# Performance work log

Measured on AMD Instinct MI355X. Metric: run time of the kernel, lower is better.

Reference implementation:

```python
import jax, jax.numpy as jnp
import numpy as np

G = 256        # graphs per batch
N = 256        # nodes per graph (max_n for dense padding)
D = 256        # node_hidden_dim
H = 8          # num_heads
EPS = 1e-5


def _layer_norm(h, g, b):
    mu = jnp.mean(h, axis=-1, keepdims=True)
    var = jnp.mean((h - mu) ** 2, axis=-1, keepdims=True)
    return (h - mu) * jax.lax.rsqrt(var + EPS) * g + b


def setup_inputs() -> dict:
    key = jax.random.key(0)
    ks = jax.random.split(key, 16)
    s = 0.02
    inp = {
        "x": jax.random.normal(ks[0], (G * N, D), dtype=jnp.float32),
        "batch": jnp.repeat(jnp.arange(G, dtype=jnp.int32), N),  # sorted segment ids
        "batch_CLS": jax.random.normal(ks[1], (G, 1, D), dtype=jnp.float32),
        "Wq": jax.random.normal(ks[2], (D, D), dtype=jnp.float32) * s,
        "bq": jnp.zeros((D,), jnp.float32),
        "Wk": jax.random.normal(ks[3], (D, D), dtype=jnp.float32) * s,
        "bk": jnp.zeros((D,), jnp.float32),
        "Wv": jax.random.normal(ks[4], (D, D), dtype=jnp.float32) * s,
        "bv": jnp.zeros((D,), jnp.float32),
        "Wo": jax.random.normal(ks[5], (D, D), dtype=jnp.float32) * s,
        "bo": jnp.zeros((D,), jnp.float32),
        "g0": jnp.ones((D,), jnp.float32),
        "beta0": jnp.zeros((D,), jnp.float32),
        "W1": jax.random.normal(ks[6], (D, 2 * D), dtype=jnp.float32) * s,
        "b1": jnp.zeros((2 * D,), jnp.float32),
        "W2": jax.random.normal(ks[7], (2 * D, D), dtype=jnp.float32) * s,
        "b2": jnp.zeros((D,), jnp.float32),
        "g1": jnp.ones((D,), jnp.float32),
        "beta1": jnp.zeros((D,), jnp.float32),
    }
    return inp


def reference(x, batch, batch_CLS, Wq, bq, Wk, bk, Wv, bv, Wo, bo,
              g0, beta0, W1, b1, W2, b2, g1, beta1):
    total = x.shape[0]
    batch = batch.astype(jnp.int32)

    # ---- to_dense_batch: scatter nodes into [G, N, D] padded tensor + mask
    counts = jax.ops.segment_sum(jnp.ones((total,), jnp.int32), batch, num_segments=G)
    start = jnp.concatenate([jnp.zeros((1,), jnp.int32), jnp.cumsum(counts)[:-1]])
    pos = jnp.arange(total, dtype=jnp.int32) - start[batch]  # position within graph
    x_dense = jnp.zeros((G, N, D), x.dtype).at[batch, pos].set(x)
    mask = jnp.zeros((G, N), bool).at[batch, pos].set(True)

    # ---- append CLS token per graph
    x_dense = jnp.concatenate([x_dense, batch_CLS], axis=1)            # [G, N+1, D]
    attn_mask = jnp.concatenate([mask, jnp.ones((G, 1), bool)], axis=1)  # [G, N+1]

    # ---- masked multi-head self-attention (split/cat pattern == head reshape)
    dh = D // H
    Q = (x_dense @ Wq + bq).reshape(G, N + 1, H, dh)
    K = (x_dense @ Wk + bk).reshape(G, N + 1, H, dh)
    V = (x_dense @ Wv + bv).reshape(G, N + 1, H, dh)
    scores = jnp.einsum('bqhd,bkhd->bhqk', Q, K) / np.sqrt(dh).astype(np.float32)
    inf_mask = jnp.where(attn_mask, 0.0, -1e9)[:, None, None, :]        # [G,1,1,N+1]
    A = jax.nn.softmax(scores + inf_mask, axis=-1)
    attn = jnp.einsum('bhqk,bkhd->bqhd', A, V).reshape(G, N + 1, D)
    attn = attn @ Wo + bo

    # ---- residual, split CLS back off, gather dense->sparse
    attn = attn + x_dense
    cls = attn[:, -1, :]                       # [G, D]
    nodes = attn[:, :-1, :][batch, pos]        # [total, D] (inverse of to_dense_batch)
    h = jnp.concatenate([nodes, cls], axis=0)  # [total + G, D]

    h = _layer_norm(h, g0, beta0)
    f = jax.nn.relu(h @ W1 + b1) @ W2 + b2
    out = _layer_norm(f + h, g1, beta1)
    return out
```

## Files before the change

kernel.cpp:

```cpp
#include <hip/hip_runtime.h>

typedef __attribute__((ext_vector_type(8))) short short8;
typedef __attribute__((ext_vector_type(8))) unsigned short ushort8;
typedef __attribute__((ext_vector_type(4))) unsigned short ushort4v;
typedef __attribute__((ext_vector_type(4))) float f32x4;
typedef unsigned short ushort;
typedef unsigned int uint;

#define QSCALE 0.17677669529663687f

__device__ __forceinline__ ushort f2bf(float f) {
  union { float f; unsigned u; } a; a.f = f;
  unsigned r = a.u + 0x7fffu + ((a.u >> 16) & 1u);
  return (ushort)(r >> 16);
}
__device__ __forceinline__ float bf2f(ushort u) {
  union { uint u; float f; } a; a.u = ((uint)u) << 16; return a.f;
}
__device__ __forceinline__ uint cvtpk(float a, float b) {
  uint r; asm("v_cvt_pk_bf16_f32 %0, %1, %2" : "=v"(r) : "v"(a), "v"(b)); return r;
}

__device__ __forceinline__ void gload16(const void* g, void* l) {
  __builtin_amdgcn_global_load_lds((const __attribute__((address_space(1))) void*)g,
                                   (__attribute__((address_space(3))) void*)l, 16, 0, 0);
}

__device__ __forceinline__ uint xcd_swz(uint hwid, uint nwg) {
  const uint q8 = nwg >> 3, r8 = nwg & 7;
  const uint xcd = hwid & 7, i8 = hwid >> 3;
  return (xcd < r8 ? xcd * (q8 + 1) : r8 * (q8 + 1) + (xcd - r8) * q8) + i8;
}

__global__ __launch_bounds__(256) void seg_start_k(const int* __restrict__ batch,
                                                   int* __restrict__ start) {
  const int i = blockIdx.x * 256 + threadIdx.x;
  const int b = batch[i];
  if (i == 0 || batch[i - 1] != b) start[b] = i;
  if (i == 0) start[256] = 65536;
}

__global__ __launch_bounds__(256) void prep_w_k(
    const float* __restrict__ Wq, const float* __restrict__ Wk,
    const float* __restrict__ Wv, const float* __restrict__ Wo,
    const float* __restrict__ W1, const float* __restrict__ W2,
    ushort* __restrict__ Wt) {
  const int w = blockIdx.y;
  const float* src; ushort* dst; int Kd, Nd; float sc = 1.0f;
  switch (w) {
    case 0: src = Wq; dst = Wt;          Kd = 256; Nd = 256; sc = QSCALE; break;
    case 1: src = Wk; dst = Wt + 65536;  Kd = 256; Nd = 256; break;
    case 2: src = Wv; dst = Wt + 131072; Kd = 256; Nd = 256; break;
    case 3: src = Wo; dst = Wt + 196608; Kd = 256; Nd = 256; break;
    case 4: src = W1; dst = Wt + 262144; Kd = 256; Nd = 512; break;
    default: src = W2; dst = Wt + 393216; Kd = 512; Nd = 256; break;
  }
  const int e = blockIdx.x * 256 + threadIdx.x;
  if (e < Kd * Nd) {
    const int k = e / Nd, n = e - k * Nd;
    dst[n * Kd + k] = f2bf(src[e] * sc);
  }
}

__global__ __launch_bounds__(256) void pack_xd_k(
    const float* __restrict__ x, const float* __restrict__ cls,
    const int* __restrict__ start, ushort* __restrict__ xd) {
  const size_t idx = (((size_t)blockIdx.x << 8) + threadIdx.x) << 3;
  const int row = (int)(idx >> 8);
  const int col = (int)(idx & 255);
  const int g = row / 257, n = row - g * 257;
  const int sg = start[g], cn = start[g + 1] - sg;
  float4 a, b;
  if (n < cn) {
    const float* src = x + (((size_t)(sg + n)) << 8) + col;
    a = ((const float4*)src)[0]; b = ((const float4*)src)[1];
  } else if (n == 256) {
    const float* src = cls + (((size_t)g) << 8) + col;
    a = ((const float4*)src)[0]; b = ((const float4*)src)[1];
  } else {
    a.x = a.y = a.z = a.w = 0.f; b = a;
  }
  ushort8 o;
  o[0] = f2bf(a.x); o[1] = f2bf(a.y); o[2] = f2bf(a.z); o[3] = f2bf(a.w);
  o[4] = f2bf(b.x); o[5] = f2bf(b.y); o[6] = f2bf(b.z); o[7] = f2bf(b.w);
  *(ushort8*)(xd + idx) = o;
}

template<int EPI>
__device__ __forceinline__ void gemm_a_body(
    const ushort* __restrict__ A, const ushort* __restrict__ Bt,
    int N, int K,
    const float* __restrict__ b0, const float* __restrict__ b1, const float* __restrict__ b2,
    ushort* __restrict__ o0, ushort* __restrict__ o1, ushort* __restrict__ o2,
    float* __restrict__ of32, const ushort* __restrict__ resid,
    const int* __restrict__ start) {
  __shared__ __align__(16) char As[16384];
  __shared__ __align__(16) char Bs[16384];
  const int tid = threadIdx.x, lane = tid & 63, wid = tid >> 6;
  const int hi = lane >> 4, lc = lane & 15;
  const int wm = wid >> 1, wn = wid & 1;

  const uint nx = gridDim.x, ny = gridDim.y;
  const uint hwid = blockIdx.y * nx + blockIdx.x;
  const uint wg = xcd_swz(hwid, nx * ny);
  const int bx = wg / ny, by = wg % ny;

  const int m0 = bx * 128;
  const int z = (EPI == 0) ? (by >> 1) : 0;
  const int ncol0 = (EPI == 0) ? (by & 1) * 128 : by * 128;
  const ushort* Bz = (EPI == 0) ? Bt + (size_t)z * 65536 : Bt;
  const float* bias = (EPI == 0) ? (z == 0 ? b0 : (z == 1 ? b1 : b2)) : b0;
  const float bmul = (EPI == 0 && z == 0) ? QSCALE : 1.0f;
  ushort* obf = (EPI == 0) ? (z == 0 ? o0 : (z == 1 ? o1 : o2)) : o0;

  f32x4 acc[4][4];
#pragma unroll
  for (int a = 0; a < 4; ++a)
#pragma unroll
    for (int b = 0; b < 4; ++b) acc[a][b] = (f32x4)0.0f;

  for (int kt = 0; kt < K; kt += 64) {
#pragma unroll
    for (int r = 0; r < 4; ++r) {
      const int L = (r * 256 + tid) * 16;
      const int row = L >> 7;
      const int cb = (L & 127) ^ ((row & 7) << 4);
      gload16(A + (size_t)(m0 + row) * K + kt + (cb >> 1), As + L);
    }
#pragma unroll
    for (int r = 0; r < 4; ++r) {
      const int L = (r * 256 + tid) * 16;
      const int row = L >> 7;
      const int cb = (L & 127) ^ ((row & 7) << 4);
      gload16(Bz + (size_t)(ncol0 + row) * K + kt + (cb >> 1), Bs + L);
    }
    asm volatile("s_waitcnt vmcnt(0)" ::: "memory");
    __syncthreads();
#pragma unroll
    for (int ks = 0; ks < 2; ++ks) {
      short8 af[4], bfr[4];
      const int cB = (ks * 32 + hi * 8) * 2;
#pragma unroll
      for (int t = 0; t < 4; ++t) {
        const int rA = wm * 64 + t * 16 + lc;
        af[t] = *(const short8*)(As + (rA << 7) + (cB ^ ((rA & 7) << 4)));
        const int rB = wn * 64 + t * 16 + lc;
        bfr[t] = *(const short8*)(Bs + (rB << 7) + (cB ^ ((rB & 7) << 4)));
      }
#pragma unroll
      for (int mt = 0; mt < 4; ++mt)
#pragma unroll
        for (int nt = 0; nt < 4; ++nt)
          acc[mt][nt] = __builtin_amdgcn_mfma_f32_16x16x32_bf16(af[mt], bfr[nt], acc[mt][nt], 0, 0, 0);
    }
    __syncthreads();
  }

#pragma unroll
  for (int mt = 0; mt < 4; ++mt)
#pragma unroll
    for (int i = 0; i < 4; ++i) {
      const int m = m0 + wm * 64 + mt * 16 + hi * 4 + i;
      size_t r2 = (size_t)m;
      bool wr = true;
      if constexpr (EPI == 4) {
        const int gg = m / 257, nr = m - gg * 257;
        const int sg = start[gg], cn = start[gg + 1] - sg;
        if (nr < cn) r2 = (size_t)(sg + nr);
        else if (nr == 256) r2 = (size_t)(65536 + gg);
        else wr = false;
      }
#pragma unroll
      for (int nt = 0; nt < 4; ++nt) {
        const int n = ncol0 + wn * 64 + nt * 16 + lc;
        if constexpr (EPI == 0) {
          obf[(size_t)m * N + n] = f2bf(acc[mt][nt][i] + bias[n] * bmul);
        } else if constexpr (EPI == 2) {
          obf[(size_t)m * N + n] = f2bf(fmaxf(acc[mt][nt][i] + bias[n], 0.0f));
        } else if constexpr (EPI == 4) {
          if (wr) {
            const float v = acc[mt][nt][i] + bias[n] + bf2f(resid[((size_t)m << 8) + n]);
            obf[(r2 << 8) + n] = f2bf(v);
          }
        } else {
          const float v = acc[mt][nt][i] + bias[n] + bf2f(resid[((size_t)m << 8) + n]);
          of32[((size_t)m << 8) + n] = v;
        }
      }
    }
}

__global__ __launch_bounds__(256) void gemm_qkv(
    const ushort* A, const ushort* Bt, const float* bq, const float* bk, const float* bv,
    ushort* Q, ushort* K, ushort* V) {
  gemm_a_body<0>(A, Bt, 256, 256, bq, bk, bv, Q, K, V, nullptr, nullptr, nullptr);
}
__global__ __launch_bounds__(256) void gemm_ffn1(
    const ushort* A, const ushort* Bt, const float* b1, ushort* t16) {
  gemm_a_body<2>(A, Bt, 512, 256, b1, nullptr, nullptr, t16, nullptr, nullptr,
                 nullptr, nullptr, nullptr);
}
__global__ __launch_bounds__(256) void gemm_wo(
    const ushort* A, const ushort* Bt, const float* bo,
    ushort* hpre16, const ushort* resid, const int* start) {
  gemm_a_body<4>(A, Bt, 256, 256, bo, nullptr, nullptr, hpre16, nullptr, nullptr,
                 nullptr, resid, start);
}
__global__ __launch_bounds__(256) void gemm_ffn2(
    const ushort* A, const ushort* Bt, const float* b2,
    float* out, const ushort* resid) {
  gemm_a_body<5>(A, Bt, 256, 512, b2, nullptr, nullptr, nullptr, nullptr, nullptr,
                 out, resid, nullptr);
}

template<int IN_BF, int OUT_BF>
__global__ __launch_bounds__(512) void ln_k(const void* __restrict__ in,
                                            const float* __restrict__ gamma,
                                            const float* __restrict__ beta,
                                            void* __restrict__ outp) {
  const int lane = threadIdx.x & 63, wid = threadIdx.x >> 6;
  const size_t r = (size_t)blockIdx.x * 8 + wid;
  float f[4];
  if constexpr (IN_BF) {
    const ushort4v v = *(const ushort4v*)((const ushort*)in + (r << 8) + lane * 4);
    f[0] = bf2f(v[0]); f[1] = bf2f(v[1]); f[2] = bf2f(v[2]); f[3] = bf2f(v[3]);
  } else {
    const float4 v = *(const float4*)((const float*)in + (r << 8) + lane * 4);
    f[0] = v.x; f[1] = v.y; f[2] = v.z; f[3] = v.w;
  }
  float s = (f[0] + f[1]) + (f[2] + f[3]);
  float ss = (f[0] * f[0] + f[1] * f[1]) + (f[2] * f[2] + f[3] * f[3]);
#pragma unroll
  for (int m = 1; m < 64; m <<= 1) {
    s += __shfl_xor(s, m); ss += __shfl_xor(ss, m);
  }
  const float mu = s * (1.0f / 256.0f);
  const float rs = rsqrtf(ss * (1.0f / 256.0f) - mu * mu + 1e-5f);
  const float4 gv = *(const float4*)(gamma + lane * 4);
  const float4 bv = *(const float4*)(beta + lane * 4);
  float o[4];
  o[0] = (f[0] - mu) * rs * gv.x + bv.x;
  o[1] = (f[1] - mu) * rs * gv.y + bv.y;
  o[2] = (f[2] - mu) * rs * gv.z + bv.z;
  o[3] = (f[3] - mu) * rs * gv.w + bv.w;
  if constexpr (OUT_BF) {
    ushort4v u;
    u[0] = f2bf(o[0]); u[1] = f2bf(o[1]); u[2] = f2bf(o[2]); u[3] = f2bf(o[3]);
    *(ushort4v*)((ushort*)outp + (r << 8) + lane * 4) = u;
  } else {
    float4 u; u.x = o[0]; u.y = o[1]; u.z = o[2]; u.w = o[3];
    *(float4*)((float*)outp + (r << 8) + lane * 4) = u;
  }
}

#define KSTR 40
#define VSTR 296
#define OSTR 40
__global__ __launch_bounds__(512) void attn_k(
    const ushort* __restrict__ Q, const ushort* Kb,
    const ushort* __restrict__ Vb, const int* __restrict__ start,
    ushort* O) {
  __shared__ __align__(16) ushort Ks[272 * KSTR];
  __shared__ __align__(16) ushort Vt[32 * VSTR];
  __shared__ __align__(16) ushort Ot[8][16 * OSTR];
  const int tid = threadIdx.x, lane = tid & 63, wid = tid >> 6;
  const int hi = lane >> 4, lo = lane & 15;
  const uint wg = xcd_swz(blockIdx.x, 2048);
  const int g = wg >> 3, h = wg & 7;
  const int cnt = start[g + 1] - start[g];
  const size_t base = ((size_t)g * 257) * 256 + h * 32;

  for (int n = tid; n < 272; n += 512) {
    const bool rv = (n < cnt) || (n == 256);
    if (n < 257 && rv) {
      const ushort* src = Kb + base + ((size_t)n << 8);
#pragma unroll
      for (int j = 0; j < 4; ++j)
        *(ushort8*)(Ks + n * KSTR + j * 8) = *(const ushort8*)(src + j * 8);
    } else {
      const ushort8 zz = (ushort8)0;
#pragma unroll
      for (int j = 0; j < 4; ++j) *(ushort8*)(Ks + n * KSTR + j * 8) = zz;
    }
  }
  for (int it = tid; it < 1152; it += 512) {
    const int n = it >> 2, d0 = (it & 3) * 8;
    const bool rv = (n < cnt) || (n == 256);
    ushort8 v8;
    if (n < 257 && rv) v8 = *(const ushort8*)(Vb + base + ((size_t)n << 8) + d0);
    else v8 = (ushort8)0;
#pragma unroll
    for (int j = 0; j < 8; ++j) Vt[(d0 + j) * VSTR + n] = v8[j];
  }
  __syncthreads();

  for (int qt = wid; qt < 17; qt += 8) {
    const int qr = qt * 16 + lo;
    const int qc = qr < 257 ? qr : 256;
    const short8 qf = *(const short8*)(Q + base + ((size_t)qc << 8) + hi * 8);

    float den = -(float)(271 - cnt);
    uint ds_[17][2];
#pragma unroll
    for (int kt = 0; kt < 17; ++kt) {
      const short8 kf = *(const short8*)(Ks + (kt * 16 + lo) * KSTR + hi * 8);
      const f32x4 st = __builtin_amdgcn_mfma_f32_16x16x32_bf16(kf, qf, (f32x4)0.0f, 0, 0, 0);
      const float e0 = __expf(st[0]), e1 = __expf(st[1]);
      const float e2 = __expf(st[2]), e3 = __expf(st[3]);
      den += (e0 + e1) + (e2 + e3);
      ds_[kt][0] = cvtpk(e0, e1);
      ds_[kt][1] = cvtpk(e2, e3);
    }
    den += __shfl_xor(den, 16);
    den += __shfl_xor(den, 32);
    const float inv = 1.0f / den;

    f32x4 ot0 = (f32x4)0.0f, ot1 = (f32x4)0.0f;
#pragma unroll
    for (int ks = 0; ks < 9; ++ks) {
      union { uint u[4]; short8 s8; } pb;
#pragma unroll
      for (int jp = 0; jp < 4; ++jp) {
        const int sl = lo | ((((hi & 1) << 1) | (jp >> 1)) << 4);
        if (ks < 8) {
          const uint a = (uint)__shfl((int)ds_[2 * ks][jp & 1], sl);
          const uint b = (uint)__shfl((int)ds_[2 * ks + 1][jp & 1], sl);
          pb.u[jp] = (hi < 2) ? a : b;
        } else {
          const uint a = (uint)__shfl((int)ds_[16][jp & 1], sl);
          pb.u[jp] = (hi < 2) ? a : 0u;
        }
      }
      const short8 va0 = *(const short8*)(Vt + lo * VSTR + ks * 32 + hi * 8);
      const short8 va1 = *(const short8*)(Vt + (16 + lo) * VSTR + ks * 32 + hi * 8);
      ot0 = __builtin_amdgcn_mfma_f32_16x16x32_bf16(va0, pb.s8, ot0, 0, 0, 0);
      ot1 = __builtin_amdgcn_mfma_f32_16x16x32_bf16(va1, pb.s8, ot1, 0, 0, 0);
    }

    {
      const uint w0 = cvtpk(ot0[0] * inv, ot0[1] * inv);
      const uint w1 = cvtpk(ot0[2] * inv, ot0[3] * inv);
      const uint w2 = cvtpk(ot1[0] * inv, ot1[1] * inv);
      const uint w3 = cvtpk(ot1[2] * inv, ot1[3] * inv);
      ushort* ob = Ot[wid] + lo * OSTR + hi * 4;
      *(uint*)(ob + 0) = w0;
      *(uint*)(ob + 2) = w1;
      *(uint*)(ob + 16) = w2;
      *(uint*)(ob + 18) = w3;
    }
    asm volatile("s_waitcnt lgkmcnt(0)" ::: "memory");
    __builtin_amdgcn_sched_barrier(0);
    {
      const int r = lane >> 2;
      const int q2 = qt * 16 + r;
      const ushort8 ov = *(const ushort8*)(Ot[wid] + r * OSTR + (lane & 3) * 8);
      if (q2 < 257)
        *(ushort8*)(O + base + ((size_t)q2 << 8) + (lane & 3) * 8) = ov;
    }
    __builtin_amdgcn_sched_barrier(0);
  }
}

extern "C" void kernel_launch(void* const* d_in, const int* in_sizes, int n_in,
                              void* d_out, int out_size, void* d_ws, size_t ws_size,
                              hipStream_t stream) {
  (void)in_sizes; (void)n_in; (void)out_size; (void)ws_size;
  const float* x     = (const float*)d_in[0];
  const int*   batch = (const int*)d_in[1];
  const float* cls   = (const float*)d_in[2];
  const float* Wq    = (const float*)d_in[3];
  const float* bq    = (const float*)d_in[4];
  const float* Wk    = (const float*)d_in[5];
  const float* bk    = (const float*)d_in[6];
  const float* Wv    = (const float*)d_in[7];
  const float* bv    = (const float*)d_in[8];
  const float* Wo    = (const float*)d_in[9];
  const float* bo    = (const float*)d_in[10];
  const float* g0    = (const float*)d_in[11];
  const float* beta0 = (const float*)d_in[12];
  const float* W1    = (const float*)d_in[13];
  const float* b1    = (const float*)d_in[14];
  const float* W2    = (const float*)d_in[15];
  const float* b2    = (const float*)d_in[16];
  const float* g1    = (const float*)d_in[17];
  const float* beta1 = (const float*)d_in[18];

  char* ws = (char*)d_ws;
  int*    start = (int*)ws;
  ushort* Wt    = (ushort*)(ws + 4096);
  char*   sbase = ws + 1052672;
  ushort* Qb    = (ushort*)(sbase);
  ushort* Kb2   = (ushort*)(sbase + 33685504);
  ushort* Vb2   = (ushort*)(sbase + 67371008);
  ushort* hpre16 = Qb;
  ushort* h16   = Vb2;
  ushort* tmid  = Qb;
  ushort* xd    = (ushort*)d_out;
  float*  out   = (float*)d_out;

  seg_start_k<<<256, 256, 0, stream>>>(batch, start);
  prep_w_k<<<dim3(512, 6), 256, 0, stream>>>(Wq, Wk, Wv, Wo, W1, W2, Wt);
  pack_xd_k<<<8224, 256, 0, stream>>>(x, cls, start, xd);
  gemm_qkv<<<dim3(514, 6), 256, 0, stream>>>(xd, Wt, bq, bk, bv, Qb, Kb2, Vb2);
  attn_k<<<2048, 512, 0, stream>>>(Qb, Kb2, Vb2, start, Kb2);
  gemm_wo<<<dim3(514, 2), 256, 0, stream>>>(Kb2, Wt + 196608, bo, hpre16, xd, start);
  ln_k<1, 1><<<8224, 512, 0, stream>>>(hpre16, g0, beta0, h16);
  gemm_ffn1<<<dim3(514, 4), 256, 0, stream>>>(h16, Wt + 262144, b1, tmid);
  gemm_ffn2<<<dim3(514, 2), 256, 0, stream>>>(tmid, Wt + 393216, b2, out, h16);
  ln_k<0, 0><<<8224, 512, 0, stream>>>(out, g1, beta1, out);
}
```

Before: 270.0 us.

## Stage softmax probabilities through LDS in attention; store FFN2 output as bf16

The attention kernel no longer keeps all 17 exp tiles in registers and rebuilds the PV operand with cross-lane shuffles. It now writes bf16 probabilities to a per-wave LDS buffer in three phases and reads them back as MFMA operands, which lowers register pressure and cuts shuffle traffic at the cost of LDS round-trips and waits. Separately, when the workspace is large enough, FFN2 writes its bf16 result to a scratch buffer and the final layernorm reads bf16, halving that intermediate's traffic but adding bf16 rounding before the final normalization.

```diff
diff --git a/kernel.cpp b/kernel.cpp
--- a/kernel.cpp
+++ b/kernel.cpp
@@ -4,6 +4,7 @@
 typedef __attribute__((ext_vector_type(8))) unsigned short ushort8;
 typedef __attribute__((ext_vector_type(4))) unsigned short ushort4v;
 typedef __attribute__((ext_vector_type(4))) float f32x4;
+typedef __attribute__((ext_vector_type(2))) unsigned int uint2v;
 typedef unsigned short ushort;
 typedef unsigned int uint;
 
@@ -184,7 +185,8 @@
           }
         } else {
           const float v = acc[mt][nt][i] + bias[n] + bf2f(resid[((size_t)m << 8) + n]);
-          of32[((size_t)m << 8) + n] = v;
+          if constexpr (EPI == 6) obf[((size_t)m << 8) + n] = f2bf(v);
+          else of32[((size_t)m << 8) + n] = v;
         }
       }
     }
@@ -211,6 +213,12 @@
     float* out, const ushort* resid) {
   gemm_a_body<5>(A, Bt, 256, 512, b2, nullptr, nullptr, nullptr, nullptr, nullptr,
                  out, resid, nullptr);
+}
+__global__ __launch_bounds__(256) void gemm_ffn2b(
+    const ushort* A, const ushort* Bt, const float* b2,
+    ushort* fh16, const ushort* resid) {
+  gemm_a_body<6>(A, Bt, 256, 512, b2, nullptr, nullptr, fh16, nullptr, nullptr,
+                 nullptr, resid, nullptr);
 }
 
 template<int IN_BF, int OUT_BF>
@@ -255,6 +263,7 @@
 
 #define KSTR 40
 #define VSTR 296
+#define PSTR 104
 #define OSTR 40
 __global__ __launch_bounds__(512) void attn_k(
     const ushort* __restrict__ Q, const ushort* Kb,
@@ -262,7 +271,7 @@
     ushort* O) {
   __shared__ __align__(16) ushort Ks[272 * KSTR];
   __shared__ __align__(16) ushort Vt[32 * VSTR];
-  __shared__ __align__(16) ushort Ot[8][16 * OSTR];
+  __shared__ __align__(16) ushort Pb[8][16 * PSTR];
   const int tid = threadIdx.x, lane = tid & 63, wid = tid >> 6;
   const int hi = lane >> 4, lo = lane & 15;
   const uint wg = xcd_swz(blockIdx.x, 2048);
@@ -298,51 +307,52 @@
     const int qr = qt * 16 + lo;
     const int qc = qr < 257 ? qr : 256;
     const short8 qf = *(const short8*)(Q + base + ((size_t)qc << 8) + hi * 8);
+    ushort* Pw = Pb[wid];
 
     float den = -(float)(271 - cnt);
-    uint ds_[17][2];
-#pragma unroll
-    for (int kt = 0; kt < 17; ++kt) {
-      const short8 kf = *(const short8*)(Ks + (kt * 16 + lo) * KSTR + hi * 8);
-      const f32x4 st = __builtin_amdgcn_mfma_f32_16x16x32_bf16(kf, qf, (f32x4)0.0f, 0, 0, 0);
-      const float e0 = __expf(st[0]), e1 = __expf(st[1]);
-      const float e2 = __expf(st[2]), e3 = __expf(st[3]);
-      den += (e0 + e1) + (e2 + e3);
-      ds_[kt][0] = cvtpk(e0, e1);
-      ds_[kt][1] = cvtpk(e2, e3);
-    }
+    f32x4 ot0 = (f32x4)0.0f, ot1 = (f32x4)0.0f;
+
+#pragma unroll
+    for (int ph = 0; ph < 3; ++ph) {
+      const int nb = ph * 96;
+      const int ktEnd = (ph == 2) ? 17 : ph * 6 + 6;
+#pragma unroll
+      for (int kt = ph * 6; kt < ktEnd; ++kt) {
+        const short8 kf = *(const short8*)(Ks + (kt * 16 + lo) * KSTR + hi * 8);
+        const f32x4 st = __builtin_amdgcn_mfma_f32_16x16x32_bf16(kf, qf, (f32x4)0.0f, 0, 0, 0);
+        const float e0 = __expf(st[0]), e1 = __expf(st[1]);
+        const float e2 = __expf(st[2]), e3 = __expf(st[3]);
+        den += (e0 + e1) + (e2 + e3);
+        uint2v w; w[0] = cvtpk(e0, e1); w[1] = cvtpk(e2, e3);
+        *(uint2v*)(Pw + lo * PSTR + (kt * 16 + hi * 4 - nb)) = w;
+      }
+      if (ph == 2) {
+        uint2v z0; z0[0] = 0u; z0[1] = 0u;
+        *(uint2v*)(Pw + lo * PSTR + (80 + hi * 4)) = z0;
+      }
+      asm volatile("s_waitcnt lgkmcnt(0)" ::: "memory");
+      __builtin_amdgcn_sched_barrier(0);
+#pragma unroll
+      for (int ks = ph * 3; ks < ph * 3 + 3; ++ks) {
+        const short8 pbf = *(const short8*)(Pw + lo * PSTR + (ks * 32 + hi * 8 - nb));
+        const short8 va0 = *(const short8*)(Vt + lo * VSTR + ks * 32 + hi * 8);
+        const short8 va1 = *(const short8*)(Vt + (16 + lo) * VSTR + ks * 32 + hi * 8);
+        ot0 = __builtin_amdgcn_mfma_f32_16x16x32_bf16(va0, pbf, ot0, 0, 0, 0);
+        ot1 = __builtin_amdgcn_mfma_f32_16x16x32_bf16(va1, pbf, ot1, 0, 0, 0);
+      }
+      __builtin_amdgcn_sched_barrier(0);
+    }
+
     den += __shfl_xor(den, 16);
     den += __shfl_xor(den, 32);
     const float inv = 1.0f / den;
-
-    f32x4 ot0 = (f32x4)0.0f, ot1 = (f32x4)0.0f;
-#pragma unroll
-    for (int ks = 0; ks < 9; ++ks) {
-      union { uint u[4]; short8 s8; } pb;
-#pragma unroll
-      for (int jp = 0; jp < 4; ++jp) {
-        const int sl = lo | ((((hi & 1) << 1) | (jp >> 1)) << 4);
-        if (ks < 8) {
-          const uint a = (uint)__shfl((int)ds_[2 * ks][jp & 1], sl);
-          const uint b = (uint)__shfl((int)ds_[2 * ks + 1][jp & 1], sl);
-          pb.u[jp] = (hi < 2) ? a : b;
-        } else {
-          const uint a = (uint)__shfl((int)ds_[16][jp & 1], sl);
-          pb.u[jp] = (hi < 2) ? a : 0u;
-        }
-      }
-      const short8 va0 = *(const short8*)(Vt + lo * VSTR + ks * 32 + hi * 8);
-      const short8 va1 = *(const short8*)(Vt + (16 + lo) * VSTR + ks * 32 + hi * 8);
-      ot0 = __builtin_amdgcn_mfma_f32_16x16x32_bf16(va0, pb.s8, ot0, 0, 0, 0);
-      ot1 = __builtin_amdgcn_mfma_f32_16x16x32_bf16(va1, pb.s8, ot1, 0, 0, 0);
-    }
 
     {
       const uint w0 = cvtpk(ot0[0] * inv, ot0[1] * inv);
       const uint w1 = cvtpk(ot0[2] * inv, ot0[3] * inv);
       const uint w2 = cvtpk(ot1[0] * inv, ot1[1] * inv);
       const uint w3 = cvtpk(ot1[2] * inv, ot1[3] * inv);
-      ushort* ob = Ot[wid] + lo * OSTR + hi * 4;
+      ushort* ob = Pw + lo * OSTR + hi * 4;
       *(uint*)(ob + 0) = w0;
       *(uint*)(ob + 2) = w1;
       *(uint*)(ob + 16) = w2;
@@ -353,7 +363,7 @@
     {
       const int r = lane >> 2;
       const int q2 = qt * 16 + r;
-      const ushort8 ov = *(const ushort8*)(Ot[wid] + r * OSTR + (lane & 3) * 8);
+      const ushort8 ov = *(const ushort8*)(Pw + r * OSTR + (lane & 3) * 8);
       if (q2 < 257)
         *(ushort8*)(O + base + ((size_t)q2 << 8) + (lane & 3) * 8) = ov;
     }
@@ -364,7 +374,7 @@
 extern "C" void kernel_launch(void* const* d_in, const int* in_sizes, int n_in,
                               void* d_out, int out_size, void* d_ws, size_t ws_size,
                               hipStream_t stream) {
-  (void)in_sizes; (void)n_in; (void)out_size; (void)ws_size;
+  (void)in_sizes; (void)n_in; (void)out_size;
   const float* x     = (const float*)d_in[0];
   const int*   batch = (const int*)d_in[1];
   const float* cls   = (const float*)d_in[2];
@@ -392,11 +402,13 @@
   ushort* Qb    = (ushort*)(sbase);
   ushort* Kb2   = (ushort*)(sbase + 33685504);
   ushort* Vb2   = (ushort*)(sbase + 67371008);
+  ushort* fh16  = (ushort*)(sbase + 101056512);
   ushort* hpre16 = Qb;
   ushort* h16   = Vb2;
   ushort* tmid  = Qb;
   ushort* xd    = (ushort*)d_out;
   float*  out   = (float*)d_out;
+  const bool big_ws = ws_size >= (size_t)135794688;
 
   seg_start_k<<<256, 256, 0, stream>>>(batch, start);
   prep_w_k<<<dim3(512, 6), 256, 0, stream>>>(Wq, Wk, Wv, Wo, W1, W2, Wt);
@@ -406,6 +418,11 @@
   gemm_wo<<<dim3(514, 2), 256, 0, stream>>>(Kb2, Wt + 196608, bo, hpre16, xd, start);
   ln_k<1, 1><<<8224, 512, 0, stream>>>(hpre16, g0, beta0, h16);
   gemm_ffn1<<<dim3(514, 4), 256, 0, stream>>>(h16, Wt + 262144, b1, tmid);
-  gemm_ffn2<<<dim3(514, 2), 256, 0, stream>>>(tmid, Wt + 393216, b2, out, h16);
-  ln_k<0, 0><<<8224, 512, 0, stream>>>(out, g1, beta1, out);
-}
+  if (big_ws) {
+    gemm_ffn2b<<<dim3(514, 2), 256, 0, stream>>>(tmid, Wt + 393216, b2, fh16, h16);
+    ln_k<1, 0><<<8224, 512, 0, stream>>>(fh16, g1, beta1, out);
+  } else {
+    gemm_ffn2<<<dim3(514, 2), 256, 0, stream>>>(tmid, Wt + 393216, b2, out, h16);
+    ln_k<0, 0><<<8224, 512, 0, stream>>>(out, g1, beta1, out);
+  }
+}
```

Result: no change. 265.3 us (-1.7%).
